# Optimization experiments

Measured on AMD Instinct MI355X. Metric: run time of the kernel, lower is better.

Reference implementation:

```python
import jax, jax.numpy as jnp
import numpy as np

N, L, D = 32768, 15, 256
VOCAB, SCORE_MAX = 27, 100


def setup_inputs() -> dict:
    key = jax.random.key(0)
    ks = jax.random.split(key, 16)
    inp = {
        'words': jax.random.randint(ks[0], (N, L), 0, VOCAB, dtype=jnp.int32),
        'rows': jax.random.randint(ks[1], (N,), 0, L, dtype=jnp.int32),
        'cols': jax.random.randint(ks[2], (N,), 0, L, dtype=jnp.int32),
        'dirs': jax.random.randint(ks[3], (N,), 0, 2, dtype=jnp.int32),
        'scores': jax.random.randint(ks[4], (N,), 0, 150, dtype=jnp.int32),
        'letter_emb': jax.random.normal(ks[5], (VOCAB, D), jnp.float32),
        'positional': jax.random.normal(ks[6], (L, D), jnp.float32),
        'Wq': jax.random.normal(ks[7], (D, D), jnp.float32) / np.sqrt(D),
        'bq': jax.random.normal(ks[8], (D,), jnp.float32) * 0.01,
        'Wk': jax.random.normal(ks[9], (D, D), jnp.float32) / np.sqrt(D),
        'bk': jax.random.normal(ks[10], (D,), jnp.float32) * 0.01,
        'Wv': jax.random.normal(ks[11], (D, D), jnp.float32) / np.sqrt(D),
        'bv': jax.random.normal(ks[12], (D,), jnp.float32) * 0.01,
        'row_emb': jax.random.normal(ks[13], (L, D), jnp.float32),
        'col_emb': jax.random.normal(ks[14], (L, D), jnp.float32),
        'dir_emb': jax.random.normal(ks[15], (2, D), jnp.float32),
        'score_emb': jax.random.normal(jax.random.fold_in(key, 99), (SCORE_MAX, D), jnp.float32),
    }
    return inp


def reference(words, rows, cols, dirs, scores, letter_emb, positional, Wq, bq, Wk, bk, Wv, bv, row_emb, col_emb, dir_emb, score_emb):
    # WordEncoder: letter embedding + positional, then single-head self-attention, sum over positions
    emb = letter_emb[words] + positional[None, :, :]            # [N, L, D]
    q = emb @ Wq.T + bq                                          # [N, L, D]
    k = emb @ Wk.T + bk
    v = emb @ Wv.T + bv
    att = jax.nn.softmax(jnp.einsum('nld,nmd->nlm', q, k), axis=-1)  # [N, L, L]
    word = jnp.einsum('nlm,nmd->nd', att, v)                     # (att @ v).sum(axis=1) -> [N, D]
    # VectorEncoder
    vector = row_emb[rows] + col_emb[cols] + dir_emb[dirs]       # [N, D]
    # score embedding (clamped to score_max - 1)
    score_v = score_emb[jnp.minimum(scores, SCORE_MAX - 1)]      # [N, D]
    # original computes word_enc(move.word) twice (word + ordered) -> 2 * word
    return 2.0 * word + vector + score_v
```

## Files before the change

### kernel.cpp

```cpp
#include <hip/hip_runtime.h>
#include <hip/hip_bf16.h>

#define NMOV 32768
#define LW 15
#define DIM 256
#define NVOC 27
#define NR 405
#define GSH 408
#define MPB 16

__device__ __forceinline__ float b2f(unsigned short u) {
    return __uint_as_float(((unsigned int)u) << 16);
}
__device__ __forceinline__ unsigned short f2bu(float x) {
    __hip_bfloat16 h = __float2bfloat16(x);
    return *reinterpret_cast<unsigned short*>(&h);
}

__device__ const unsigned char PAIR_LUT[120] = {
    0x00,
    0x10,0x11,
    0x20,0x21,0x22,
    0x30,0x31,0x32,0x33,
    0x40,0x41,0x42,0x43,0x44,
    0x50,0x51,0x52,0x53,0x54,0x55,
    0x60,0x61,0x62,0x63,0x64,0x65,0x66,
    0x70,0x71,0x72,0x73,0x74,0x75,0x76,0x77,
    0x80,0x81,0x82,0x83,0x84,0x85,0x86,0x87,0x88,
    0x90,0x91,0x92,0x93,0x94,0x95,0x96,0x97,0x98,0x99,
    0xA0,0xA1,0xA2,0xA3,0xA4,0xA5,0xA6,0xA7,0xA8,0xA9,0xAA,
    0xB0,0xB1,0xB2,0xB3,0xB4,0xB5,0xB6,0xB7,0xB8,0xB9,0xBA,0xBB,
    0xC0,0xC1,0xC2,0xC3,0xC4,0xC5,0xC6,0xC7,0xC8,0xC9,0xCA,0xCB,0xCC,
    0xD0,0xD1,0xD2,0xD3,0xD4,0xD5,0xD6,0xD7,0xD8,0xD9,0xDA,0xDB,0xDC,0xDD,
    0xE0,0xE1,0xE2,0xE3,0xE4,0xE5,0xE6,0xE7,0xE8,0xE9,0xEA,0xEB,0xEC,0xED,0xEE
};

__global__ __launch_bounds__(256) void qkv_gemm(
    const float* __restrict__ le, const float* __restrict__ pos,
    const float* __restrict__ Wq, const float* __restrict__ bq,
    const float* __restrict__ Wk, const float* __restrict__ bk,
    const float* __restrict__ Wv, const float* __restrict__ bv,
    const float* __restrict__ row_emb, const float* __restrict__ col_emb,
    const float* __restrict__ dir_emb, const float* __restrict__ score_emb,
    float* __restrict__ QT, float* __restrict__ KT,
    __hip_bfloat16* __restrict__ VT, __hip_bfloat16* __restrict__ EPI)
{
    const int t = threadIdx.x;
    if (blockIdx.x >= 312) {
        int idx = (blockIdx.x - 312) * 1024 + t * 4;
        float4 v;
        if (idx < 15 * 256)       v = *(const float4*)&row_emb[idx];
        else if (idx < 30 * 256)  v = *(const float4*)&col_emb[idx - 15 * 256];
        else if (idx < 32 * 256)  v = *(const float4*)&dir_emb[idx - 30 * 256];
        else                      v = *(const float4*)&score_emb[idx - 32 * 256];
        ushort4 o;
        o.x = f2bu(v.x); o.y = f2bu(v.y); o.z = f2bu(v.z); o.w = f2bu(v.w);
        *(ushort4*)((unsigned short*)EPI + idx) = o;
        return;
    }

    __shared__ float Ash[32][68];
    __shared__ float Bsh[32][68];
    const int bx = blockIdx.x % 24;
    const int by = blockIdx.x / 24;
    const int r0 = by * 32;
    const int mat = bx >> 3;
    const int nb  = (bx & 7) * 32;
    const float* W  = (mat == 0) ? Wq : (mat == 1) ? Wk : Wv;
    const float* bb = (mat == 0) ? bq : (mat == 1) ? bk : bv;

    const int ti = t >> 4, tj = t & 15;
    float acc00 = 0.f, acc01 = 0.f, acc10 = 0.f, acc11 = 0.f;

    for (int k0 = 0; k0 < DIM; k0 += 64) {
        #pragma unroll
        for (int s = 0; s < 2; ++s) {
            int slot = s * 256 + t;
            int row = slot >> 4, c4 = slot & 15;
            int r = r0 + row;
            float4 va = make_float4(0.f, 0.f, 0.f, 0.f);
            if (r < NR) {
                int c = r / 15, l = r - c * 15;
                float4 lv = *(const float4*)&le[c * DIM + k0 + c4 * 4];
                float4 pv = *(const float4*)&pos[l * DIM + k0 + c4 * 4];
                va = make_float4(lv.x + pv.x, lv.y + pv.y, lv.z + pv.z, lv.w + pv.w);
            }
            *(float4*)&Ash[row][c4 * 4] = va;
            float4 vb = *(const float4*)&W[(nb + row) * DIM + k0 + c4 * 4];
            *(float4*)&Bsh[row][c4 * 4] = vb;
        }
        __syncthreads();
        #pragma unroll 4
        for (int kk = 0; kk < 64; kk += 4) {
            float4 a0 = *(const float4*)&Ash[2 * ti][kk];
            float4 a1 = *(const float4*)&Ash[2 * ti + 1][kk];
            float4 b0 = *(const float4*)&Bsh[tj][kk];
            float4 b1 = *(const float4*)&Bsh[tj + 16][kk];
            acc00 += a0.x * b0.x + a0.y * b0.y + a0.z * b0.z + a0.w * b0.w;
            acc01 += a0.x * b1.x + a0.y * b1.y + a0.z * b1.z + a0.w * b1.w;
            acc10 += a1.x * b0.x + a1.y * b0.y + a1.z * b0.z + a1.w * b0.w;
            acc11 += a1.x * b1.x + a1.y * b1.y + a1.z * b1.z + a1.w * b1.w;
        }
        __syncthreads();
    }

    const int c0 = nb + tj, c1 = nb + tj + 16;
    const float bias0 = bb[c0], bias1 = bb[c1];
    #pragma unroll
    for (int rr = 0; rr < 2; ++rr) {
        int r = r0 + 2 * ti + rr;
        if (r < NR) {
            float v0 = (rr == 0 ? acc00 : acc10) + bias0;
            float v1 = (rr == 0 ? acc01 : acc11) + bias1;
            if (mat == 0) {
                QT[r * DIM + c0] = v0; QT[r * DIM + c1] = v1;
            } else if (mat == 1) {
                KT[r * DIM + c0] = v0; KT[r * DIM + c1] = v1;
            } else {
                VT[r * DIM + c0] = __float2bfloat16(v0);
                VT[r * DIM + c1] = __float2bfloat16(v1);
            }
        }
    }
}

__global__ __launch_bounds__(256) void h_matrix(
    const float* __restrict__ QT, const float* __restrict__ KT,
    float2* __restrict__ H)
{
    __shared__ float Qi[16][68], Ki[16][68], Qj[16][68], Kj[16][68];

    int rem = blockIdx.x, bi = 0, cnt = 26;
    while (rem >= cnt) { rem -= cnt; ++bi; --cnt; }
    const int bj = bi + rem;
    const int i0 = bi * 16, j0 = bj * 16;
    const int t = threadIdx.x;
    const int ti = t >> 4, tj = t & 15;

    float acc_ij = 0.f, acc_ji = 0.f;

    for (int k0 = 0; k0 < DIM; k0 += 64) {
        #pragma unroll
        for (int s = 0; s < 4; ++s) {
            int slot = s * 256 + t;
            int tile = slot >> 8;
            int r    = (slot >> 4) & 15;
            int c4   = slot & 15;
            int grow = (tile < 2) ? (i0 + r) : (j0 + r);
            const float* src = (tile == 0 || tile == 2) ? QT : KT;
            float4 v = (grow < NR)
                ? *(const float4*)&src[grow * DIM + k0 + c4 * 4]
                : make_float4(0.f, 0.f, 0.f, 0.f);
            float* dst = (tile == 0) ? &Qi[r][c4 * 4]
                       : (tile == 1) ? &Ki[r][c4 * 4]
                       : (tile == 2) ? &Qj[r][c4 * 4] : &Kj[r][c4 * 4];
            *(float4*)dst = v;
        }
        __syncthreads();
        #pragma unroll 4
        for (int k = 0; k < 64; k += 4) {
            float4 qi = *(const float4*)&Qi[ti][k];
            float4 kj = *(const float4*)&Kj[tj][k];
            float4 qj = *(const float4*)&Qj[ti][k];
            float4 ki = *(const float4*)&Ki[tj][k];
            acc_ij += qi.x * kj.x + qi.y * kj.y + qi.z * kj.z + qi.w * kj.w;
            acc_ji += qj.x * ki.x + qj.y * ki.y + qj.z * ki.z + qj.w * ki.w;
        }
        __syncthreads();
    }

    Qi[ti][tj] = acc_ij;
    Ki[ti][tj] = acc_ji;
    __syncthreads();
    const float t_ij = Qi[tj][ti];
    const float t_ji = Ki[tj][ti];

    const int i1 = i0 + ti, j1 = j0 + tj;
    if (i1 < NR && j1 < NR) H[i1 * GSH + j1] = make_float2(acc_ij, t_ji);
    const int i2 = j0 + ti, j2 = i0 + tj;
    if (i2 < NR && j2 < NR) H[i2 * GSH + j2] = make_float2(acc_ji, t_ij);
}

__global__ __launch_bounds__(256) void moves_kernel(
    const int* __restrict__ words, const int* __restrict__ rowsI,
    const int* __restrict__ colsI, const int* __restrict__ dirsI,
    const int* __restrict__ scoresI,
    const float2* __restrict__ H, const __hip_bfloat16* __restrict__ VT,
    const __hip_bfloat16* __restrict__ EPI,
    float* __restrict__ out)
{
    __shared__ float S[MPB][LW][17];
    __shared__ int   rIdx[MPB][16];
    __shared__ float csum[MPB][16];
    __shared__ int   meta[MPB][4];
    const int base = blockIdx.x * MPB;
    const int t  = threadIdx.x;
    const int w  = t >> 6;
    const int ln = t & 63;
    const int hw = t >> 5;
    const int j  = t & 31;

    const int mv0 = hw * 2, mv1 = mv0 + 1;
    const int* w0 = words + (base + mv0) * LW;
    const int* w1 = words + (base + mv1) * LW;
    int ll[4], mm[4];
    float2 h0[4], h1[4];
    #pragma unroll
    for (int k = 0; k < 4; ++k) {
        int p = j + 32 * k;
        if (p < 120) {
            int lm = PAIR_LUT[p];
            ll[k] = lm >> 4; mm[k] = lm & 15;
            int rl0 = w0[ll[k]] * LW + ll[k];
            int rm0 = w0[mm[k]] * LW + mm[k];
            int rl1 = w1[ll[k]] * LW + ll[k];
            int rm1 = w1[mm[k]] * LW + mm[k];
            h0[k] = H[(size_t)rl0 * GSH + rm0];
            h1[k] = H[(size_t)rl1 * GSH + rm1];
        }
    }

    if (ln < 60) {
        int mvl = ln / 15, row = ln - mvl * 15;
        int mv = w * 4 + mvl;
        rIdx[mv][row] = words[(base + mv) * LW + row] * LW + row;
    }
    if (ln < 16) {
        int mvl = ln >> 2, f = ln & 3;
        int n = base + w * 4 + mvl;
        int v = (f == 0) ? rowsI[n] : (f == 1) ? 15 + colsI[n]
              : (f == 2) ? 30 + dirsI[n] : 32 + min(scoresI[n], 99);
        meta[w * 4 + mvl][f] = v;
    }

    #pragma unroll
    for (int k = 0; k < 4; ++k) {
        int p = j + 32 * k;
        if (p < 120) {
            S[mv0][ll[k]][mm[k]] = h0[k].x;
            S[mv0][mm[k]][ll[k]] = h0[k].y;
            S[mv1][ll[k]][mm[k]] = h1[k].x;
            S[mv1][mm[k]][ll[k]] = h1[k].y;
        }
    }
    __builtin_amdgcn_wave_barrier();

    if (ln < 60) {
        int mvl = ln / 15, row = ln - mvl * 15;
        int mv = w * 4 + mvl;
        float s[LW];
        #pragma unroll
        for (int m = 0; m < LW; ++m) s[m] = S[mv][row][m];
        float mx = s[0];
        #pragma unroll
        for (int m = 1; m < LW; ++m) mx = fmaxf(mx, s[m]);
        float sum = 0.f;
        #pragma unroll
        for (int m = 0; m < LW; ++m) { s[m] = __expf(s[m] - mx); sum += s[m]; }
        float inv = 1.0f / sum;
        #pragma unroll
        for (int m = 0; m < LW; ++m) S[mv][row][m] = s[m] * inv;
    }
    __builtin_amdgcn_wave_barrier();

    if (ln < 60) {
        int mvl = ln / 15, col = ln - mvl * 15;
        int mv = w * 4 + mvl;
        float acc = 0.f;
        #pragma unroll
        for (int l = 0; l < LW; ++l) acc += S[mv][l][col];
        csum[mv][col] = acc;
    }
    __builtin_amdgcn_wave_barrier();

    const int d0 = ln * 4;
    const unsigned short* VT16 = (const unsigned short*)VT;
    const unsigned short* EP16 = (const unsigned short*)EPI;
    #pragma unroll 1
    for (int s2 = 0; s2 < 4; ++s2) {
        const int i = w * 4 + s2;
        const int n = base + i;
        ushort4 re = *(const ushort4*)(EP16 + meta[i][0] * DIM + d0);
        ushort4 ce = *(const ushort4*)(EP16 + meta[i][1] * DIM + d0);
        ushort4 de = *(const ushort4*)(EP16 + meta[i][2] * DIM + d0);
        ushort4 se = *(const ushort4*)(EP16 + meta[i][3] * DIM + d0);
        ushort4 va[8];
        #pragma unroll
        for (int m = 0; m < 8; ++m)
            va[m] = *(const ushort4*)(VT16 + (size_t)rIdx[i][m] * DIM + d0);
        float wx = 0.f, wy = 0.f, wz = 0.f, ww = 0.f;
        #pragma unroll
        for (int m = 0; m < 8; ++m) {
            float c = csum[i][m];
            wx += c * b2f(va[m].x); wy += c * b2f(va[m].y);
            wz += c * b2f(va[m].z); ww += c * b2f(va[m].w);
        }
        ushort4 vb[7];
        #pragma unroll
        for (int m = 0; m < 7; ++m)
            vb[m] = *(const ushort4*)(VT16 + (size_t)rIdx[i][8 + m] * DIM + d0);
        #pragma unroll
        for (int m = 0; m < 7; ++m) {
            float c = csum[i][8 + m];
            wx += c * b2f(vb[m].x); wy += c * b2f(vb[m].y);
            wz += c * b2f(vb[m].z); ww += c * b2f(vb[m].w);
        }
        float4 res;
        res.x = 2.f * wx + b2f(re.x) + b2f(ce.x) + b2f(de.x) + b2f(se.x);
        res.y = 2.f * wy + b2f(re.y) + b2f(ce.y) + b2f(de.y) + b2f(se.y);
        res.z = 2.f * wz + b2f(re.z) + b2f(ce.z) + b2f(de.z) + b2f(se.z);
        res.w = 2.f * ww + b2f(re.w) + b2f(ce.w) + b2f(de.w) + b2f(se.w);
        *(float4*)&out[(size_t)n * DIM + d0] = res;
    }
}

extern "C" void kernel_launch(void* const* d_in, const int* in_sizes, int n_in,
                              void* d_out, int out_size, void* d_ws, size_t ws_size,
                              hipStream_t stream)
{
    const int*   words      = (const int*)d_in[0];
    const int*   rowsI      = (const int*)d_in[1];
    const int*   colsI      = (const int*)d_in[2];
    const int*   dirsI      = (const int*)d_in[3];
    const int*   scoresI    = (const int*)d_in[4];
    const float* letter_emb = (const float*)d_in[5];
    const float* positional = (const float*)d_in[6];
    const float* Wq         = (const float*)d_in[7];
    const float* bq         = (const float*)d_in[8];
    const float* Wk         = (const float*)d_in[9];
    const float* bk         = (const float*)d_in[10];
    const float* Wv         = (const float*)d_in[11];
    const float* bv         = (const float*)d_in[12];
    const float* row_emb    = (const float*)d_in[13];
    const float* col_emb    = (const float*)d_in[14];
    const float* dir_emb    = (const float*)d_in[15];
    const float* score_emb  = (const float*)d_in[16];
    float* out = (float*)d_out;

    float*  QT = (float*)d_ws;
    float*  KT = QT + NR * DIM;
    float2* Hm = (float2*)(KT + NR * DIM);
    __hip_bfloat16* VT  = (__hip_bfloat16*)((char*)Hm + (size_t)NR * GSH * sizeof(float2));
    __hip_bfloat16* EPI = VT + (size_t)NR * DIM;

    qkv_gemm<<<345, 256, 0, stream>>>(letter_emb, positional, Wq, bq, Wk, bk,
                                      Wv, bv, row_emb, col_emb, dir_emb,
                                      score_emb, QT, KT, VT, EPI);
    h_matrix<<<351, 256, 0, stream>>>(QT, KT, Hm);
    moves_kernel<<<NMOV / MPB, 256, 0, stream>>>(words, rowsI, colsI, dirsI,
                                                 scoresI, Hm, VT, EPI, out);
}
```

Before: 65.23 us.

## Split K dimension across two blocks with atomic accumulation in QKV and H kernels

Doubles the grid of the QKV projection and H-matrix kernels by splitting the 256-long reduction into two halves, each block atomically adding its partial sum into a workspace zeroed by a memset. V is now kept in fp32 so it can be atomically accumulated, and the moves kernel reads fp32 V instead of bf16. The goal is more parallelism in the small prologue kernels. The cost is an extra memset launch, atomic traffic, and doubled V gather bandwidth in the main kernel.

```diff
diff --git a/kernel.cpp b/kernel.cpp
--- a/kernel.cpp
+++ b/kernel.cpp
@@ -43,11 +43,11 @@
     const float* __restrict__ row_emb, const float* __restrict__ col_emb,
     const float* __restrict__ dir_emb, const float* __restrict__ score_emb,
     float* __restrict__ QT, float* __restrict__ KT,
-    __hip_bfloat16* __restrict__ VT, __hip_bfloat16* __restrict__ EPI)
+    float* __restrict__ VTF, __hip_bfloat16* __restrict__ EPI)
 {
     const int t = threadIdx.x;
-    if (blockIdx.x >= 312) {
-        int idx = (blockIdx.x - 312) * 1024 + t * 4;
+    if (blockIdx.x >= 624) {
+        int idx = (blockIdx.x - 624) * 1024 + t * 4;
         float4 v;
         if (idx < 15 * 256)       v = *(const float4*)&row_emb[idx];
         else if (idx < 30 * 256)  v = *(const float4*)&col_emb[idx - 15 * 256];
@@ -61,8 +61,11 @@
 
     __shared__ float Ash[32][68];
     __shared__ float Bsh[32][68];
-    const int bx = blockIdx.x % 24;
-    const int by = blockIdx.x / 24;
+    const int gb = blockIdx.x >> 1;
+    const int kh = blockIdx.x & 1;
+    const int koff = kh * 128;
+    const int bx = gb % 24;
+    const int by = gb / 24;
     const int r0 = by * 32;
     const int mat = bx >> 3;
     const int nb  = (bx & 7) * 32;
@@ -72,7 +75,7 @@
     const int ti = t >> 4, tj = t & 15;
     float acc00 = 0.f, acc01 = 0.f, acc10 = 0.f, acc11 = 0.f;
 
-    for (int k0 = 0; k0 < DIM; k0 += 64) {
+    for (int k0 = koff; k0 < koff + 128; k0 += 64) {
         #pragma unroll
         for (int s = 0; s < 2; ++s) {
             int slot = s * 256 + t;
@@ -105,21 +108,17 @@
     }
 
     const int c0 = nb + tj, c1 = nb + tj + 16;
-    const float bias0 = bb[c0], bias1 = bb[c1];
+    const float bias0 = (kh == 0) ? bb[c0] : 0.f;
+    const float bias1 = (kh == 0) ? bb[c1] : 0.f;
+    float* D = (mat == 0) ? QT : (mat == 1) ? KT : VTF;
     #pragma unroll
     for (int rr = 0; rr < 2; ++rr) {
         int r = r0 + 2 * ti + rr;
         if (r < NR) {
             float v0 = (rr == 0 ? acc00 : acc10) + bias0;
             float v1 = (rr == 0 ? acc01 : acc11) + bias1;
-            if (mat == 0) {
-                QT[r * DIM + c0] = v0; QT[r * DIM + c1] = v1;
-            } else if (mat == 1) {
-                KT[r * DIM + c0] = v0; KT[r * DIM + c1] = v1;
-            } else {
-                VT[r * DIM + c0] = __float2bfloat16(v0);
-                VT[r * DIM + c1] = __float2bfloat16(v1);
-            }
+            atomicAdd(&D[r * DIM + c0], v0);
+            atomicAdd(&D[r * DIM + c1], v1);
         }
     }
 }
@@ -130,7 +129,10 @@
 {
     __shared__ float Qi[16][68], Ki[16][68], Qj[16][68], Kj[16][68];
 
-    int rem = blockIdx.x, bi = 0, cnt = 26;
+    const int gb = blockIdx.x >> 1;
+    const int kh = blockIdx.x & 1;
+    const int koff = kh * 128;
+    int rem = gb, bi = 0, cnt = 26;
     while (rem >= cnt) { rem -= cnt; ++bi; --cnt; }
     const int bj = bi + rem;
     const int i0 = bi * 16, j0 = bj * 16;
@@ -139,7 +141,7 @@
 
     float acc_ij = 0.f, acc_ji = 0.f;
 
-    for (int k0 = 0; k0 < DIM; k0 += 64) {
+    for (int k0 = koff; k0 < koff + 128; k0 += 64) {
         #pragma unroll
         for (int s = 0; s < 4; ++s) {
             int slot = s * 256 + t;
@@ -176,16 +178,26 @@
     const float t_ji = Ki[tj][ti];
 
     const int i1 = i0 + ti, j1 = j0 + tj;
-    if (i1 < NR && j1 < NR) H[i1 * GSH + j1] = make_float2(acc_ij, t_ji);
-    const int i2 = j0 + ti, j2 = i0 + tj;
-    if (i2 < NR && j2 < NR) H[i2 * GSH + j2] = make_float2(acc_ji, t_ij);
+    if (i1 < NR && j1 < NR) {
+        float* p = (float*)&H[i1 * GSH + j1];
+        atomicAdd(p + 0, acc_ij);
+        atomicAdd(p + 1, t_ji);
+    }
+    if (bi != bj) {
+        const int i2 = j0 + ti, j2 = i0 + tj;
+        if (i2 < NR && j2 < NR) {
+            float* p = (float*)&H[i2 * GSH + j2];
+            atomicAdd(p + 0, acc_ji);
+            atomicAdd(p + 1, t_ij);
+        }
+    }
 }
 
 __global__ __launch_bounds__(256) void moves_kernel(
     const int* __restrict__ words, const int* __restrict__ rowsI,
     const int* __restrict__ colsI, const int* __restrict__ dirsI,
     const int* __restrict__ scoresI,
-    const float2* __restrict__ H, const __hip_bfloat16* __restrict__ VT,
+    const float2* __restrict__ H, const float* __restrict__ VTF,
     const __hip_bfloat16* __restrict__ EPI,
     float* __restrict__ out)
 {
@@ -274,7 +286,6 @@
     __builtin_amdgcn_wave_barrier();
 
     const int d0 = ln * 4;
-    const unsigned short* VT16 = (const unsigned short*)VT;
     const unsigned short* EP16 = (const unsigned short*)EPI;
     #pragma unroll 1
     for (int s2 = 0; s2 < 4; ++s2) {
@@ -284,26 +295,26 @@
         ushort4 ce = *(const ushort4*)(EP16 + meta[i][1] * DIM + d0);
         ushort4 de = *(const ushort4*)(EP16 + meta[i][2] * DIM + d0);
         ushort4 se = *(const ushort4*)(EP16 + meta[i][3] * DIM + d0);
-        ushort4 va[8];
+        float4 va[8];
         #pragma unroll
         for (int m = 0; m < 8; ++m)
-            va[m] = *(const ushort4*)(VT16 + (size_t)rIdx[i][m] * DIM + d0);
+            va[m] = *(const float4*)(VTF + (size_t)rIdx[i][m] * DIM + d0);
         float wx = 0.f, wy = 0.f, wz = 0.f, ww = 0.f;
         #pragma unroll
         for (int m = 0; m < 8; ++m) {
             float c = csum[i][m];
-            wx += c * b2f(va[m].x); wy += c * b2f(va[m].y);
-            wz += c * b2f(va[m].z); ww += c * b2f(va[m].w);
-        }
-        ushort4 vb[7];
+            wx += c * va[m].x; wy += c * va[m].y;
+            wz += c * va[m].z; ww += c * va[m].w;
+        }
+        float4 vb[7];
         #pragma unroll
         for (int m = 0; m < 7; ++m)
-            vb[m] = *(const ushort4*)(VT16 + (size_t)rIdx[i][8 + m] * DIM + d0);
+            vb[m] = *(const float4*)(VTF + (size_t)rIdx[i][8 + m] * DIM + d0);
         #pragma unroll
         for (int m = 0; m < 7; ++m) {
             float c = csum[i][8 + m];
-            wx += c * b2f(vb[m].x); wy += c * b2f(vb[m].y);
-            wz += c * b2f(vb[m].z); ww += c * b2f(vb[m].w);
+            wx += c * vb[m].x; wy += c * vb[m].y;
+            wz += c * vb[m].z; ww += c * vb[m].w;
         }
         float4 res;
         res.x = 2.f * wx + b2f(re.x) + b2f(ce.x) + b2f(de.x) + b2f(se.x);
@@ -337,16 +348,20 @@
     const float* score_emb  = (const float*)d_in[16];
     float* out = (float*)d_out;
 
-    float*  QT = (float*)d_ws;
-    float*  KT = QT + NR * DIM;
-    float2* Hm = (float2*)(KT + NR * DIM);
-    __hip_bfloat16* VT  = (__hip_bfloat16*)((char*)Hm + (size_t)NR * GSH * sizeof(float2));
-    __hip_bfloat16* EPI = VT + (size_t)NR * DIM;
-
-    qkv_gemm<<<345, 256, 0, stream>>>(letter_emb, positional, Wq, bq, Wk, bk,
+    float*  QT  = (float*)d_ws;
+    float*  KT  = QT + NR * DIM;
+    float2* Hm  = (float2*)(KT + NR * DIM);
+    float*  VTF = (float*)((char*)Hm + (size_t)NR * GSH * sizeof(float2));
+    __hip_bfloat16* EPI = (__hip_bfloat16*)(VTF + NR * DIM);
+
+    size_t zero_bytes = (size_t)(2 * NR * DIM * 4) + (size_t)NR * GSH * 8
+                      + (size_t)NR * DIM * 4;
+    hipMemsetAsync(d_ws, 0, zero_bytes, stream);
+
+    qkv_gemm<<<657, 256, 0, stream>>>(letter_emb, positional, Wq, bq, Wk, bk,
                                       Wv, bv, row_emb, col_emb, dir_emb,
-                                      score_emb, QT, KT, VT, EPI);
-    h_matrix<<<351, 256, 0, stream>>>(QT, KT, Hm);
+                                      score_emb, QT, KT, VTF, EPI);
+    h_matrix<<<702, 256, 0, stream>>>(QT, KT, Hm);
     moves_kernel<<<NMOV / MPB, 256, 0, stream>>>(words, rowsI, colsI, dirsI,
-                                                 scoresI, Hm, VT, EPI, out);
-}
+                                                 scoresI, Hm, VTF, EPI, out);
+}
```

New measurement: 74.56 us. +14.3%, slower.
